# Optimization experiments

Measured on AMD Instinct MI355X. Metric: run time of the kernel, lower is better.

## Reference

```python
import jax, jax.numpy as jnp
import numpy as np

B, S, HIDDEN = 2, 1024, 2048
N_HEADS, N_KV_HEADS, HEAD_DIM = 32, 8, 64
GROUP = N_HEADS // N_KV_HEADS  # 4
ROPE_THETA = 10000.0


def rotate_half(x):
    half = x.shape[-1] // 2
    return jnp.concatenate((-x[..., half:], x[..., :half]), axis=-1)


def setup_inputs() -> dict:
    key = jax.random.key(0)
    ks = jax.random.split(key, 5)
    hidden_state = jax.random.normal(ks[0], (B, S, HIDDEN), jnp.float32)
    attention_mask = jnp.ones((B, S), jnp.float32)
    # RoPE tables, shape (S, HEAD_DIM)
    inv_freq = 1.0 / (ROPE_THETA ** (jnp.arange(0, HEAD_DIM, 2, dtype=jnp.float32) / HEAD_DIM))
    freqs = jnp.outer(jnp.arange(S, dtype=jnp.float32), inv_freq)
    emb = jnp.concatenate([freqs, freqs], axis=-1)
    cos, sin = jnp.cos(emb), jnp.sin(emb)
    scale = 0.02
    wq = jax.random.normal(ks[1], (HIDDEN, N_HEADS * HEAD_DIM), jnp.float32) * scale
    wk = jax.random.normal(ks[2], (HIDDEN, N_KV_HEADS * HEAD_DIM), jnp.float32) * scale
    wv = jax.random.normal(ks[3], (HIDDEN, N_KV_HEADS * HEAD_DIM), jnp.float32) * scale
    wo = jax.random.normal(ks[4], (N_HEADS * HEAD_DIM, HIDDEN), jnp.float32) * scale
    return {"hidden_state": hidden_state, "attention_mask": attention_mask,
            "cos": cos, "sin": sin, "wq": wq, "wk": wk, "wv": wv, "wo": wo}


def reference(hidden_state, attention_mask, cos, sin, wq, wk, wv, wo):
    b, s, _ = hidden_state.shape

    def split_heads(x):  # (B,S,n*D) -> (n,B,S,D), matching movedim(-2, 0)
        return jnp.moveaxis(x.reshape(b, s, -1, HEAD_DIM), -2, 0)

    q = split_heads(hidden_state @ wq)   # (H, B, S, D)
    k = split_heads(hidden_state @ wk)   # (KV, B, S, D)
    v = split_heads(hidden_state @ wv)   # (KV, B, S, D)

    q = q * cos + rotate_half(q) * sin
    k = k * cos + rotate_half(k) * sin

    # GQA: repeat_interleave K/V heads to match query heads
    k = jnp.repeat(k, GROUP, axis=0)     # (H, B, S, D)
    v = jnp.repeat(v, GROUP, axis=0)

    scores = jnp.einsum('hbqd,hbkd->hbqk', q, k) / jnp.sqrt(jnp.float32(HEAD_DIM))

    # causal + padding mask bias: 0 where tril(mask)==1, -inf elsewhere
    m = jnp.tril(jnp.broadcast_to(attention_mask[:, None, :], (b, s, s)))  # (B,S,S)
    bias = jnp.where((1.0 - m) != 0.0, -jnp.inf, 0.0)
    scores = scores + bias               # (H,B,S,S) + (B,S,S)

    attn = jax.nn.softmax(scores, axis=-1)
    ctx = jnp.einsum('hbqk,hbkd->hbqd', attn, v)
    ctx = jnp.moveaxis(ctx, 0, -2).reshape(b, s, -1)  # (B,S,H*D)
    out = ctx @ wo
    return (out, jnp.swapaxes(attn, 0, 1))  # attention.transpose(0,1) -> (B,H,S,S)
```

## Files before the change

kernel.cpp:

```cpp
#include <hip/hip_runtime.h>


typedef unsigned short u16;
typedef unsigned int   u32;
typedef __attribute__((ext_vector_type(4))) float  f32x4;
typedef __attribute__((ext_vector_type(8))) __bf16 bf16x8;

static __device__ __forceinline__ u16 f2b(float f) {
  u32 u = __builtin_bit_cast(u32, f);
  u = u + 0x7fffu + ((u >> 16) & 1u);
  return (u16)(u >> 16);
}
static __device__ __forceinline__ float b2f(u16 h) {
  u32 u = ((u32)h) << 16;
  return __builtin_bit_cast(float, u);
}

#define GLL16(gp, lp)                                                         \
  __builtin_amdgcn_global_load_lds(                                           \
      (__attribute__((address_space(1))) u32*)(gp),                           \
      (__attribute__((address_space(3))) u32*)(lp), 16, 0, 0)

__global__ __launch_bounds__(256) void cvt_kernel(const float* __restrict__ in,
                                                  u16* __restrict__ out, int n4) {
  int i = blockIdx.x * 256 + threadIdx.x;
  if (i >= n4) return;
  float4 v = ((const float4*)in)[i];
  ushort4 o;
  o.x = f2b(v.x); o.y = f2b(v.y); o.z = f2b(v.z); o.w = f2b(v.w);
  ((ushort4*)out)[i] = o;
}

__global__ __launch_bounds__(256) void tconv_kernel(const float* __restrict__ in,
                                                    u16* __restrict__ out,
                                                    int K, int N) {
  __shared__ float t[64][65];
  int k0 = blockIdx.x * 64, n0 = blockIdx.y * 64;
  int c = threadIdx.x & 63, r0 = threadIdx.x >> 6;
#pragma unroll
  for (int i = 0; i < 16; ++i) {
    int r = r0 + i * 4;
    t[r][c] = in[(size_t)(k0 + r) * N + n0 + c];
  }
  __syncthreads();
#pragma unroll
  for (int i = 0; i < 16; ++i) {
    int r = r0 + i * 4;
    out[(size_t)(n0 + r) * K + k0 + c] = f2b(t[c][r]);
  }
}

__global__ __launch_bounds__(256) void vtrans_kernel(const u16* __restrict__ vb,
                                                     u16* __restrict__ vt) {
  __shared__ u16 t[64][65];
  int s0 = blockIdx.x * 64;
  int g = blockIdx.y;
  int b = g >> 3, kvh = g & 7;
  int c = threadIdx.x & 63, r0 = threadIdx.x >> 6;
#pragma unroll
  for (int i = 0; i < 16; ++i) {
    int r = r0 + i * 4;
    t[r][c] = vb[(size_t)(b * 1024 + s0 + r) * 512 + kvh * 64 + c];
  }
  __syncthreads();
#pragma unroll
  for (int i = 0; i < 16; ++i) {
    int r = r0 + i * 4;
    vt[((size_t)g * 64 + r) * 1024 + s0 + c] = t[c][r];
  }
}

__global__ __launch_bounds__(256) void rope_kernel(u16* __restrict__ buf,
                                                   const float* __restrict__ cosT,
                                                   const float* __restrict__ sinT,
                                                   int nhl) {
  int idx = blockIdx.x * 256 + threadIdx.x;
  int dp = idx & 31;
  int rest = idx >> 5;
  int hh = rest & ((1 << nhl) - 1);
  int t = rest >> nhl;
  int s = t & 1023;
  size_t base = ((size_t)t << (nhl + 6)) + ((size_t)hh << 6);
  float q0 = b2f(buf[base + dp]);
  float q1 = b2f(buf[base + dp + 32]);
  float c0 = cosT[s * 64 + dp],      s0v = sinT[s * 64 + dp];
  float c1 = cosT[s * 64 + dp + 32], s1v = sinT[s * 64 + dp + 32];
  buf[base + dp]      = f2b(q0 * c0 - q1 * s0v);
  buf[base + dp + 32] = f2b(q1 * c1 + q0 * s1v);
}

template <int EPI>
__global__ __launch_bounds__(256) void gemm_kernel(
    const u16* __restrict__ A, const u16* __restrict__ Bt, int K,
    u16* __restrict__ qb, u16* __restrict__ kb, u16* __restrict__ vb,
    float* __restrict__ out) {
  __shared__ u16 As[128 * 64];
  __shared__ u16 Bs[128 * 64];
  const int tid = threadIdx.x;
  const int w = tid >> 6, l = tid & 63;
  const int wr = w >> 1, wc = w & 1;
  const int lg = l >> 4, ll = l & 15;
  const int l8 = l >> 3, lc = l & 7;
  const int m0 = blockIdx.x * 128, n0 = blockIdx.y * 128;

  f32x4 acc[4][4] = {};

  const int nkt = K >> 6;
  for (int kt = 0; kt < nkt; ++kt) {
    __syncthreads();
#pragma unroll
    for (int i = 0; i < 4; ++i) {
      int r0 = w * 32 + i * 8;
      int row = r0 + l8;
      int cc = lc ^ (row & 7);
      GLL16(A  + (size_t)(m0 + row) * K + kt * 64 + cc * 8, &As[r0 * 64]);
      GLL16(Bt + (size_t)(n0 + row) * K + kt * 64 + cc * 8, &Bs[r0 * 64]);
    }
    __syncthreads();
#pragma unroll
    for (int kc = 0; kc < 2; ++kc) {
      int cblk = kc * 4 + lg;
      bf16x8 af[4], bfr[4];
#pragma unroll
      for (int mi = 0; mi < 4; ++mi) {
        int row = wr * 64 + mi * 16 + ll;
        af[mi] = *(const bf16x8*)&As[row * 64 + ((cblk ^ (row & 7)) * 8)];
      }
#pragma unroll
      for (int ni = 0; ni < 4; ++ni) {
        int row = wc * 64 + ni * 16 + ll;
        bfr[ni] = *(const bf16x8*)&Bs[row * 64 + ((cblk ^ (row & 7)) * 8)];
      }
#pragma unroll
      for (int mi = 0; mi < 4; ++mi)
#pragma unroll
        for (int ni = 0; ni < 4; ++ni)
          acc[mi][ni] = __builtin_amdgcn_mfma_f32_16x16x32_bf16(
              af[mi], bfr[ni], acc[mi][ni], 0, 0, 0);
    }
  }

  if constexpr (EPI == 0) {
    u16* dst; int ldc, c0;
    if (n0 < 2048)      { dst = qb; ldc = 2048; c0 = n0; }
    else if (n0 < 2560) { dst = kb; ldc = 512;  c0 = n0 - 2048; }
    else                { dst = vb; ldc = 512;  c0 = n0 - 2560; }
#pragma unroll
    for (int mi = 0; mi < 4; ++mi)
#pragma unroll
      for (int ni = 0; ni < 4; ++ni)
#pragma unroll
        for (int r = 0; r < 4; ++r) {
          int row = m0 + wr * 64 + mi * 16 + lg * 4 + r;
          int col = c0 + wc * 64 + ni * 16 + ll;
          dst[(size_t)row * ldc + col] = f2b(acc[mi][ni][r]);
        }
  } else {
#pragma unroll
    for (int mi = 0; mi < 4; ++mi)
#pragma unroll
      for (int ni = 0; ni < 4; ++ni)
#pragma unroll
        for (int r = 0; r < 4; ++r) {
          int row = m0 + wr * 64 + mi * 16 + lg * 4 + r;
          int col = n0 + wc * 64 + ni * 16 + ll;
          out[(size_t)row * 2048 + col] = acc[mi][ni][r];
        }
  }
}

__global__ __launch_bounds__(256) void attn_kernel(
    const u16* __restrict__ Qb,
    const u16* __restrict__ Kb,
    const u16* __restrict__ Vt,
    const float* __restrict__ msk,
    float* __restrict__ attn,
    u16* __restrict__ ctx) {
  __shared__ u16 Ks[64 * 64];
  __shared__ u16 Vs[64 * 64];
  __shared__ float Ps[64 * 68];
  __shared__ float Msk[1024];

  const int tid = threadIdx.x, w = tid >> 6, l = tid & 63;
  const int lg = l >> 4, ll = l & 15;
  const int l8 = l >> 3, lc = l & 7;
  const int bid = blockIdx.x;
  const int qt1 = bid & 7;
  const int h = (bid >> 3) & 31;
  const int b = bid >> 8;
  const int kvh = h >> 2;

  for (int i = tid; i < 1024; i += 256) Msk[i] = msk[b * 1024 + i];

  for (int half = 0; half < 2; ++half) {
    const int qt = half ? (15 - qt1) : qt1;
    const int qrow0 = qt * 64 + w * 16 + lg * 4;

    bf16x8 qf[2];
    {
      const u16* qp = Qb + (size_t)(b * 1024 + qt * 64 + w * 16 + ll) * 2048 +
                      h * 64 + lg * 8;
      qf[0] = *(const bf16x8*)qp;
      qf[1] = *(const bf16x8*)(qp + 32);
    }

    float l_r[4] = {0.f, 0.f, 0.f, 0.f};
    for (int kt = 0; kt <= qt; ++kt) {
      __syncthreads();
#pragma unroll
      for (int j = 0; j < 2; ++j) {
        int r0 = w * 16 + j * 8;
        int row = r0 + l8;
        int cc = lc ^ (row & 7);
        GLL16(Kb + (size_t)(b * 1024 + kt * 64 + row) * 512 + kvh * 64 + cc * 8,
              &Ks[r0 * 64]);
      }
      __syncthreads();
      f32x4 sc[4] = {};
#pragma unroll
      for (int kc = 0; kc < 2; ++kc) {
        int cblk = kc * 4 + lg;
#pragma unroll
        for (int ns = 0; ns < 4; ++ns) {
          int row = ns * 16 + ll;
          bf16x8 kf = *(const bf16x8*)&Ks[row * 64 + ((cblk ^ (row & 7)) * 8)];
          sc[ns] = __builtin_amdgcn_mfma_f32_16x16x32_bf16(qf[kc], kf, sc[ns], 0, 0, 0);
        }
      }
#pragma unroll
      for (int ns = 0; ns < 4; ++ns) {
        int col = kt * 64 + ns * 16 + ll;
        float mb = Msk[col];
#pragma unroll
        for (int r = 0; r < 4; ++r) {
          float e = __expf(sc[ns][r] * 0.125f);
          l_r[r] += (mb != 0.f && col <= qrow0 + r) ? e : 0.f;
        }
      }
    }
#pragma unroll
    for (int r = 0; r < 4; ++r) {
#pragma unroll
      for (int mm = 1; mm < 16; mm <<= 1) l_r[r] += __shfl_xor(l_r[r], mm, 64);
    }
    float rinv[4];
#pragma unroll
    for (int r = 0; r < 4; ++r) rinv[r] = 1.f / l_r[r];

    f32x4 cacc[4] = {};
    for (int kt = 0; kt <= qt; ++kt) {
      __syncthreads();
#pragma unroll
      for (int j = 0; j < 2; ++j) {
        int r0 = w * 16 + j * 8;
        int row = r0 + l8;
        int cc = lc ^ (row & 7);
        GLL16(Kb + (size_t)(b * 1024 + kt * 64 + row) * 512 + kvh * 64 + cc * 8,
              &Ks[r0 * 64]);
        GLL16(Vt + (size_t)((b * 8 + kvh) * 64 + row) * 1024 + kt * 64 + cc * 8,
              &Vs[r0 * 64]);
      }
      __syncthreads();
      f32x4 sc[4] = {};
#pragma unroll
      for (int kc = 0; kc < 2; ++kc) {
        int cblk = kc * 4 + lg;
#pragma unroll
        for (int ns = 0; ns < 4; ++ns) {
          int row = ns * 16 + ll;
          bf16x8 kf = *(const bf16x8*)&Ks[row * 64 + ((cblk ^ (row & 7)) * 8)];
          sc[ns] = __builtin_amdgcn_mfma_f32_16x16x32_bf16(qf[kc], kf, sc[ns], 0, 0, 0);
        }
      }
#pragma unroll
      for (int ns = 0; ns < 4; ++ns) {
        int col = kt * 64 + ns * 16 + ll;
        float mb = Msk[col];
#pragma unroll
        for (int r = 0; r < 4; ++r) {
          float e = __expf(sc[ns][r] * 0.125f) * rinv[r];
          float p = (mb != 0.f && col <= qrow0 + r) ? e : 0.f;
          Ps[(w * 16 + lg * 4 + r) * 68 + ns * 16 + ll] = p;
        }
      }
      __syncthreads();
      {
        size_t rowbase = ((size_t)((b * 32 + h) * 1024 + qt * 64 + w * 16));
#pragma unroll
        for (int rr = 0; rr < 4; ++rr) {
          int lr = rr * 4 + lg;
          f32x4 pv4 = *(const f32x4*)&Ps[(w * 16 + lr) * 68 + ll * 4];
          *(f32x4*)&attn[(rowbase + lr) * 1024 + kt * 64 + ll * 4] = pv4;
        }
      }
#pragma unroll
      for (int kc = 0; kc < 2; ++kc) {
        const float* pp = &Ps[(w * 16 + ll) * 68 + kc * 32 + lg * 8];
        f32x4 plo = *(const f32x4*)pp;
        f32x4 phi = *(const f32x4*)(pp + 4);
        bf16x8 pa;
        pa[0] = (__bf16)plo[0]; pa[1] = (__bf16)plo[1];
        pa[2] = (__bf16)plo[2]; pa[3] = (__bf16)plo[3];
        pa[4] = (__bf16)phi[0]; pa[5] = (__bf16)phi[1];
        pa[6] = (__bf16)phi[2]; pa[7] = (__bf16)phi[3];
        int cblk = kc * 4 + lg;
#pragma unroll
        for (int ns = 0; ns < 4; ++ns) {
          int row = ns * 16 + ll;
          bf16x8 vf = *(const bf16x8*)&Vs[row * 64 + ((cblk ^ (row & 7)) * 8)];
          cacc[ns] = __builtin_amdgcn_mfma_f32_16x16x32_bf16(pa, vf, cacc[ns], 0, 0, 0);
        }
      }
    }

#pragma unroll
    for (int ns = 0; ns < 4; ++ns)
#pragma unroll
      for (int r = 0; r < 4; ++r) {
        int tok = b * 1024 + qt * 64 + w * 16 + lg * 4 + r;
        ctx[(size_t)tok * 2048 + h * 64 + ns * 16 + ll] = f2b(cacc[ns][r]);
      }

    int c00 = (qt + 1) * 64;
    int nzf = (1024 - c00) >> 2;
    if (nzf > 0) {
      size_t rb = ((size_t)((b * 32 + h) * 1024 + qt * 64)) * 1024;
      for (int i = tid; i < 64 * nzf; i += 256) {
        int rr = i / nzf;
        int cc4 = i - rr * nzf;
        float4 z = make_float4(0.f, 0.f, 0.f, 0.f);
        *(float4*)&attn[rb + (size_t)rr * 1024 + c00 + (size_t)cc4 * 4] = z;
      }
    }
  }
}

extern "C" void kernel_launch(void* const* d_in, const int* in_sizes, int n_in,
                              void* d_out, int out_size, void* d_ws, size_t ws_size,
                              hipStream_t stream) {
  const float* hidden = (const float*)d_in[0];
  const float* mask   = (const float*)d_in[1];
  const float* cosT   = (const float*)d_in[2];
  const float* sinT   = (const float*)d_in[3];
  const float* wq     = (const float*)d_in[4];
  const float* wk     = (const float*)d_in[5];
  const float* wv     = (const float*)d_in[6];
  const float* wo     = (const float*)d_in[7];

  char* ws = (char*)d_ws;
  u16* hidbf = (u16*)(ws);
  u16* Wt    = (u16*)(ws + (8u << 20));
  u16* Qb    = (u16*)(ws + (20u << 20));
  u16* Kb    = (u16*)(ws + (28u << 20));
  u16* Vb    = (u16*)(ws + (30u << 20));
  u16* Vtg   = (u16*)(ws + (32u << 20));

  float* outp  = (float*)d_out;
  float* attnp = outp + (size_t)2 * 1024 * 2048;

  cvt_kernel<<<4096, 256, 0, stream>>>(hidden, hidbf, 1048576);
  tconv_kernel<<<dim3(32, 32), 256, 0, stream>>>(wq, Wt, 2048, 2048);
  tconv_kernel<<<dim3(32, 8), 256, 0, stream>>>(wk, Wt + (size_t)2048 * 2048, 2048, 512);
  tconv_kernel<<<dim3(32, 8), 256, 0, stream>>>(wv, Wt + (size_t)2560 * 2048, 2048, 512);
  gemm_kernel<0><<<dim3(16, 24), 256, 0, stream>>>(hidbf, Wt, 2048, Qb, Kb, Vb, nullptr);
  rope_kernel<<<8192, 256, 0, stream>>>(Qb, cosT, sinT, 5);
  rope_kernel<<<2048, 256, 0, stream>>>(Kb, cosT, sinT, 3);
  vtrans_kernel<<<dim3(16, 16), 256, 0, stream>>>(Vb, Vtg);
  tconv_kernel<<<dim3(32, 32), 256, 0, stream>>>(wo, Wt, 2048, 2048);
  attn_kernel<<<512, 256, 0, stream>>>(Qb, Kb, Vtg, mask, attnp, hidbf);
  gemm_kernel<1><<<dim3(16, 16), 256, 0, stream>>>(hidbf, Wt, 2048,
                                                   nullptr, nullptr, nullptr, outp);
}
```

Measured before the change: 469.9 us.

## Fuse RoPE into QKV GEMM epilogue and double-buffer K/V tiles in attention

The QKV GEMM epilogue now applies the rotary embedding directly. It pairs accumulator fragments ni and ni^2, which hold dimensions d and d+32, and reads cos/sin per element. This removes the two separate RoPE kernels and their bf16 read/write round trip. The attention kernel double-buffers its K and V shared-memory tiles, issuing the async global-to-LDS load for the next tile while the current one is computed, and drops one barrier per iteration. It also stores the padding mask as bytes. The epilogue now does extra scattered cos/sin loads, and the attention kernel uses more LDS, which may reduce occupancy.

After: 477.7 us. Within noise of the previous version (+1.7%).

```diff
diff --git a/kernel.cpp b/kernel.cpp
--- a/kernel.cpp
+++ b/kernel.cpp
@@ -2,6 +2,7 @@
 
 
 typedef unsigned short u16;
+typedef unsigned char  u8;
 typedef unsigned int   u32;
 typedef __attribute__((ext_vector_type(4))) float  f32x4;
 typedef __attribute__((ext_vector_type(8))) __bf16 bf16x8;
@@ -10,10 +11,6 @@
   u32 u = __builtin_bit_cast(u32, f);
   u = u + 0x7fffu + ((u >> 16) & 1u);
   return (u16)(u >> 16);
-}
-static __device__ __forceinline__ float b2f(u16 h) {
-  u32 u = ((u32)h) << 16;
-  return __builtin_bit_cast(float, u);
 }
 
 #define GLL16(gp, lp)                                                         \
@@ -70,30 +67,12 @@
   }
 }
 
-__global__ __launch_bounds__(256) void rope_kernel(u16* __restrict__ buf,
-                                                   const float* __restrict__ cosT,
-                                                   const float* __restrict__ sinT,
-                                                   int nhl) {
-  int idx = blockIdx.x * 256 + threadIdx.x;
-  int dp = idx & 31;
-  int rest = idx >> 5;
-  int hh = rest & ((1 << nhl) - 1);
-  int t = rest >> nhl;
-  int s = t & 1023;
-  size_t base = ((size_t)t << (nhl + 6)) + ((size_t)hh << 6);
-  float q0 = b2f(buf[base + dp]);
-  float q1 = b2f(buf[base + dp + 32]);
-  float c0 = cosT[s * 64 + dp],      s0v = sinT[s * 64 + dp];
-  float c1 = cosT[s * 64 + dp + 32], s1v = sinT[s * 64 + dp + 32];
-  buf[base + dp]      = f2b(q0 * c0 - q1 * s0v);
-  buf[base + dp + 32] = f2b(q1 * c1 + q0 * s1v);
-}
-
 template <int EPI>
 __global__ __launch_bounds__(256) void gemm_kernel(
     const u16* __restrict__ A, const u16* __restrict__ Bt, int K,
     u16* __restrict__ qb, u16* __restrict__ kb, u16* __restrict__ vb,
-    float* __restrict__ out) {
+    float* __restrict__ out,
+    const float* __restrict__ cosT, const float* __restrict__ sinT) {
   __shared__ u16 As[128 * 64];
   __shared__ u16 Bs[128 * 64];
   const int tid = threadIdx.x;
@@ -142,6 +121,7 @@
 
   if constexpr (EPI == 0) {
     u16* dst; int ldc, c0;
+    const bool dorope = (n0 < 2560);
     if (n0 < 2048)      { dst = qb; ldc = 2048; c0 = n0; }
     else if (n0 < 2560) { dst = kb; ldc = 512;  c0 = n0 - 2048; }
     else                { dst = vb; ldc = 512;  c0 = n0 - 2560; }
@@ -153,7 +133,15 @@
         for (int r = 0; r < 4; ++r) {
           int row = m0 + wr * 64 + mi * 16 + lg * 4 + r;
           int col = c0 + wc * 64 + ni * 16 + ll;
-          dst[(size_t)row * ldc + col] = f2b(acc[mi][ni][r]);
+          float x = acc[mi][ni][r];
+          if (dorope) {
+            int d = ni * 16 + ll;
+            int s = row & 1023;
+            float cv = cosT[s * 64 + d], sv = sinT[s * 64 + d];
+            float xp = acc[mi][ni ^ 2][r];
+            x = (ni < 2) ? (x * cv - xp * sv) : (x * cv + xp * sv);
+          }
+          dst[(size_t)row * ldc + col] = f2b(x);
         }
   } else {
 #pragma unroll
@@ -176,10 +164,10 @@
     const float* __restrict__ msk,
     float* __restrict__ attn,
     u16* __restrict__ ctx) {
-  __shared__ u16 Ks[64 * 64];
-  __shared__ u16 Vs[64 * 64];
+  __shared__ u16 Ks[2][64 * 64];
+  __shared__ u16 Vs[2][64 * 64];
   __shared__ float Ps[64 * 68];
-  __shared__ float Msk[1024];
+  __shared__ u8 Msk[1024];
 
   const int tid = threadIdx.x, w = tid >> 6, l = tid & 63;
   const int lg = l >> 4, ll = l & 15;
@@ -190,7 +178,30 @@
   const int b = bid >> 8;
   const int kvh = h >> 2;
 
-  for (int i = tid; i < 1024; i += 256) Msk[i] = msk[b * 1024 + i];
+  for (int i = tid; i < 1024; i += 256) Msk[i] = (msk[b * 1024 + i] != 0.f);
+
+#define STAGE_K(KT, BUF)                                                      \
+  {                                                                           \
+    for (int j = 0; j < 2; ++j) {                                             \
+      int r0 = w * 16 + j * 8;                                                \
+      int row = r0 + l8;                                                      \
+      int cc = lc ^ (row & 7);                                                \
+      GLL16(Kb + (size_t)(b * 1024 + (KT) * 64 + row) * 512 + kvh * 64 +      \
+                cc * 8,                                                       \
+            &Ks[BUF][r0 * 64]);                                               \
+    }                                                                         \
+  }
+#define STAGE_V(KT, BUF)                                                      \
+  {                                                                           \
+    for (int j = 0; j < 2; ++j) {                                             \
+      int r0 = w * 16 + j * 8;                                                \
+      int row = r0 + l8;                                                      \
+      int cc = lc ^ (row & 7);                                                \
+      GLL16(Vt + (size_t)((b * 8 + kvh) * 64 + row) * 1024 + (KT) * 64 +      \
+                cc * 8,                                                       \
+            &Vs[BUF][r0 * 64]);                                               \
+    }                                                                         \
+  }
 
   for (int half = 0; half < 2; ++half) {
     const int qt = half ? (15 - qt1) : qt1;
@@ -204,18 +215,13 @@
       qf[1] = *(const bf16x8*)(qp + 32);
     }
 
+    __syncthreads();
+    STAGE_K(0, 0);
     float l_r[4] = {0.f, 0.f, 0.f, 0.f};
     for (int kt = 0; kt <= qt; ++kt) {
+      const int c = kt & 1;
       __syncthreads();
-#pragma unroll
-      for (int j = 0; j < 2; ++j) {
-        int r0 = w * 16 + j * 8;
-        int row = r0 + l8;
-        int cc = lc ^ (row & 7);
-        GLL16(Kb + (size_t)(b * 1024 + kt * 64 + row) * 512 + kvh * 64 + cc * 8,
-              &Ks[r0 * 64]);
-      }
-      __syncthreads();
+      if (kt < qt) STAGE_K(kt + 1, c ^ 1);
       f32x4 sc[4] = {};
 #pragma unroll
       for (int kc = 0; kc < 2; ++kc) {
@@ -223,18 +229,18 @@
 #pragma unroll
         for (int ns = 0; ns < 4; ++ns) {
           int row = ns * 16 + ll;
-          bf16x8 kf = *(const bf16x8*)&Ks[row * 64 + ((cblk ^ (row & 7)) * 8)];
+          bf16x8 kf = *(const bf16x8*)&Ks[c][row * 64 + ((cblk ^ (row & 7)) * 8)];
           sc[ns] = __builtin_amdgcn_mfma_f32_16x16x32_bf16(qf[kc], kf, sc[ns], 0, 0, 0);
         }
       }
 #pragma unroll
       for (int ns = 0; ns < 4; ++ns) {
         int col = kt * 64 + ns * 16 + ll;
-        float mb = Msk[col];
+        bool mb = Msk[col];
 #pragma unroll
         for (int r = 0; r < 4; ++r) {
           float e = __expf(sc[ns][r] * 0.125f);
-          l_r[r] += (mb != 0.f && col <= qrow0 + r) ? e : 0.f;
+          l_r[r] += (mb && col <= qrow0 + r) ? e : 0.f;
         }
       }
     }
@@ -247,20 +253,14 @@
 #pragma unroll
     for (int r = 0; r < 4; ++r) rinv[r] = 1.f / l_r[r];
 
+    __syncthreads();
+    STAGE_K(0, 0);
+    STAGE_V(0, 0);
     f32x4 cacc[4] = {};
     for (int kt = 0; kt <= qt; ++kt) {
+      const int c = kt & 1;
       __syncthreads();
-#pragma unroll
-      for (int j = 0; j < 2; ++j) {
-        int r0 = w * 16 + j * 8;
-        int row = r0 + l8;
-        int cc = lc ^ (row & 7);
-        GLL16(Kb + (size_t)(b * 1024 + kt * 64 + row) * 512 + kvh * 64 + cc * 8,
-              &Ks[r0 * 64]);
-        GLL16(Vt + (size_t)((b * 8 + kvh) * 64 + row) * 1024 + kt * 64 + cc * 8,
-              &Vs[r0 * 64]);
-      }
-      __syncthreads();
+      if (kt < qt) { STAGE_K(kt + 1, c ^ 1); STAGE_V(kt + 1, c ^ 1); }
       f32x4 sc[4] = {};
 #pragma unroll
       for (int kc = 0; kc < 2; ++kc) {
@@ -268,22 +268,21 @@
 #pragma unroll
         for (int ns = 0; ns < 4; ++ns) {
           int row = ns * 16 + ll;
-          bf16x8 kf = *(const bf16x8*)&Ks[row * 64 + ((cblk ^ (row & 7)) * 8)];
+          bf16x8 kf = *(const bf16x8*)&Ks[c][row * 64 + ((cblk ^ (row & 7)) * 8)];
           sc[ns] = __builtin_amdgcn_mfma_f32_16x16x32_bf16(qf[kc], kf, sc[ns], 0, 0, 0);
         }
       }
 #pragma unroll
       for (int ns = 0; ns < 4; ++ns) {
         int col = kt * 64 + ns * 16 + ll;
-        float mb = Msk[col];
+        bool mb = Msk[col];
 #pragma unroll
         for (int r = 0; r < 4; ++r) {
           float e = __expf(sc[ns][r] * 0.125f) * rinv[r];
-          float p = (mb != 0.f && col <= qrow0 + r) ? e : 0.f;
+          float p = (mb && col <= qrow0 + r) ? e : 0.f;
           Ps[(w * 16 + lg * 4 + r) * 68 + ns * 16 + ll] = p;
         }
       }
-      __syncthreads();
       {
         size_t rowbase = ((size_t)((b * 32 + h) * 1024 + qt * 64 + w * 16));
 #pragma unroll
@@ -307,7 +306,7 @@
 #pragma unroll
         for (int ns = 0; ns < 4; ++ns) {
           int row = ns * 16 + ll;
-          bf16x8 vf = *(const bf16x8*)&Vs[row * 64 + ((cblk ^ (row & 7)) * 8)];
+          bf16x8 vf = *(const bf16x8*)&Vs[c][row * 64 + ((cblk ^ (row & 7)) * 8)];
           cacc[ns] = __builtin_amdgcn_mfma_f32_16x16x32_bf16(pa, vf, cacc[ns], 0, 0, 0);
         }
       }
@@ -333,6 +332,8 @@
       }
     }
   }
+#undef STAGE_K
+#undef STAGE_V
 }
 
 extern "C" void kernel_launch(void* const* d_in, const int* in_sizes, int n_in,
@@ -362,12 +363,12 @@
   tconv_kernel<<<dim3(32, 32), 256, 0, stream>>>(wq, Wt, 2048, 2048);
   tconv_kernel<<<dim3(32, 8), 256, 0, stream>>>(wk, Wt + (size_t)2048 * 2048, 2048, 512);
   tconv_kernel<<<dim3(32, 8), 256, 0, stream>>>(wv, Wt + (size_t)2560 * 2048, 2048, 512);
-  gemm_kernel<0><<<dim3(16, 24), 256, 0, stream>>>(hidbf, Wt, 2048, Qb, Kb, Vb, nullptr);
-  rope_kernel<<<8192, 256, 0, stream>>>(Qb, cosT, sinT, 5);
-  rope_kernel<<<2048, 256, 0, stream>>>(Kb, cosT, sinT, 3);
+  gemm_kernel<0><<<dim3(16, 24), 256, 0, stream>>>(hidbf, Wt, 2048, Qb, Kb, Vb,
+                                                   nullptr, cosT, sinT);
   vtrans_kernel<<<dim3(16, 16), 256, 0, stream>>>(Vb, Vtg);
   tconv_kernel<<<dim3(32, 32), 256, 0, stream>>>(wo, Wt, 2048, 2048);
   attn_kernel<<<512, 256, 0, stream>>>(Qb, Kb, Vtg, mask, attnp, hidbf);
   gemm_kernel<1><<<dim3(16, 16), 256, 0, stream>>>(hidbf, Wt, 2048,
-                                                   nullptr, nullptr, nullptr, outp);
-}
+                                                   nullptr, nullptr, nullptr, outp,
+                                                   nullptr, nullptr);
+}
```
